# Optimization experiments

Measured on AMD Instinct MI355X. Metric: run time of the kernel, lower is better.

## Reference

```python
import jax, jax.numpy as jnp
from jax import lax
import numpy as np

GAMMA = 0.1
BIG = 1e8  # finite stand-in for +inf so grads/logsumexp stay clean

# solar radius in km; HUX propagates from 21.5 Rs (WSA inner boundary) to 1 AU (215 Rs)
RS_KM = 6.957e5
R0 = 21.5 * RS_KM
R1 = 215.0 * RS_KM
NR = 200  # radial steps (CFL ~ 0.5 for v~300 km/s, T=512)


def _hux(v_in, omega):
    """HUX-f upwind radial propagation. v_in: [B,T] km/s, omega: [B] rad/s."""
    B, T = v_in.shape
    dr = (R1 - R0) / NR
    dphi = 2.0 * jnp.pi / T  # one Carrington rotation over T samples
    om = omega[:, None]

    def step(v, _):
        dv = jnp.roll(v, -1, axis=1) - v  # periodic longitude
        v_new = v + (dr * om / (jnp.maximum(v, 1.0) * dphi)) * dv
        return v_new, None

    v_out, _ = lax.scan(step, v_in, None, length=NR)
    return v_out


def _soft_dtw(x, y, gamma):
    """Soft-DTW (Cuturi & Blondel). x,y: [B,T,1]. Returns [B]."""
    B, T, _ = x.shape
    # pairwise squared-euclidean cost  [B,T,T]
    D = jnp.sum((x[:, :, None, :] - y[:, None, :, :]) ** 2, axis=-1)
    i = jnp.arange(T)

    def softmin(a, b, c):
        return -gamma * jax.nn.logsumexp(-jnp.stack([a, b, c], 0) / gamma, axis=0)

    # anti-diagonal wavefront: r1[i] = R[i, p-1-i], r2[i] = R[i, p-2-i]
    def step(carry, p):
        r2, r1 = carry
        j = p - i
        valid = (j >= 0) & (j < T)
        d = D[:, i, jnp.clip(j, 0, T - 1)]          # [B,T] cost on diag p
        n_up = jnp.concatenate([jnp.full((B, 1), BIG, D.dtype), r1[:, :-1]], 1)   # R[i-1, p-i]
        n_left = r1                                                                # R[i, p-i-1]
        n_diag = jnp.concatenate([jnp.full((B, 1), BIG, D.dtype), r2[:, :-1]], 1)  # R[i-1, p-i-1]
        r_new = d + softmin(n_up, n_left, n_diag)
        r_new = jnp.where(valid[None, :], r_new, BIG)
        return (r1, r_new), None

    r0 = jnp.full((B, T), BIG, D.dtype).at[:, 0].set(D[:, 0, 0])  # diag p=0: R[0,0]=D[0,0]
    rm1 = jnp.full((B, T), BIG, D.dtype)
    (_, r_last), _ = lax.scan(step, (rm1, r0), jnp.arange(1, 2 * T - 1))
    return r_last[:, T - 1]  # R[T-1, T-1]


def _forward(pred_map, lat_idx, omega, omni_ts):
    B, _, H, W = pred_map.shape
    v_map = pred_map[:, 0]  # [B,H,W]
    T = lat_idx.shape[1]
    # v_in[b,t] = v_map[b, t, lat_idx[b,t]]
    v_in = jnp.take_along_axis(v_map[:, :T, :], lat_idx[:, :, None], axis=2)[..., 0]
    v_out = _hux(v_in, omega)

    v_out_scaled = (v_out - 200.0) / 1000.0
    omni_scaled = (omni_ts - 200.0) / 1000.0

    dtw_raw = _soft_dtw(omni_scaled[..., None], v_out_scaled[..., None], GAMMA)
    dtw_loss = jnp.abs(dtw_raw).mean()

    diff = v_out_scaled - omni_scaled
    rmse_loss = jnp.sqrt(jnp.sum(diff ** 2))
    mae_loss = jnp.sum(jnp.abs(diff))

    pc = v_out_scaled - v_out_scaled.mean(axis=1, keepdims=True)
    tc = omni_scaled - omni_scaled.mean(axis=1, keepdims=True)
    num = jnp.sum(pc * tc, axis=1)
    den = jnp.sqrt(jnp.sum(pc ** 2, axis=1)) * jnp.sqrt(jnp.sum(tc ** 2, axis=1))
    pcc_loss = 1.0 - (num / den).mean()

    return (v_out, mae_loss, pcc_loss, dtw_loss, rmse_loss)


def setup_inputs() -> dict:
    key = jax.random.key(0)
    k1, k2, k3, k4 = jax.random.split(key, 4)
    B, T, W = 32, 512, 128
    # realistic solar-wind speeds 300-700 km/s (keeps HUX stable and loss scaling sane)
    pred_map = 300.0 + 400.0 * jax.random.uniform(k1, (B, 1, T, W), dtype=jnp.float32)
    lat_idx = jax.random.randint(k2, (B, T), 0, W)
    omega = 2.7e-6 * (0.9 + 0.2 * jax.random.uniform(k3, (B,), dtype=jnp.float32))
    omni_ts = 300.0 + 400.0 * jax.random.uniform(k4, (B, T), dtype=jnp.float32)
    return {"pred_map": pred_map, "lat_idx": lat_idx, "omega": omega, "omni_ts": omni_ts}


def reference(pred_map, lat_idx, omega, omni_ts):
    return _forward(pred_map, lat_idx, omega, omni_ts)
```

## Files before the change

kernel.cpp:

```cpp
#include <hip/hip_runtime.h>
#include <math.h>

#define TT 512
#define NB 32
#define NRSTEP 200
#define KSC 14.4269504f
#define MAGICF 0x5CA1AB1E

#define SCHR_SCALE (-KSC * 8388608.0f)
#define SCHR_OFF   1064986823.0f

typedef float float2v __attribute__((ext_vector_type(2)));

__device__ __forceinline__ float2v pk_add(float2v a, float2v b) {
    float2v d;
    asm("v_pk_add_f32 %0, %1, %2" : "=v"(d) : "v"(a), "v"(b));
    return d;
}
__device__ __forceinline__ float2v pk_mul(float2v a, float2v b) {
    float2v d;
    asm("v_pk_mul_f32 %0, %1, %2" : "=v"(d) : "v"(a), "v"(b));
    return d;
}
__device__ __forceinline__ float2v pk_fma(float2v a, float2v b, float2v c) {
    float2v d;
    asm("v_pk_fma_f32 %0, %1, %2, %3" : "=v"(d) : "v"(a), "v"(b), "v"(c));
    return d;
}

__device__ __forceinline__ float dpp_up1_f(float x) {
    return __int_as_float(__builtin_amdgcn_update_dpp(
        0, __float_as_int(x), 0x138, 0xf, 0xf, false));
}
__device__ __forceinline__ int dpp_up1_i(int x) {
    return __builtin_amdgcn_update_dpp(0, x, 0x138, 0xf, 0xf, false);
}
__device__ __forceinline__ float dpp_dn1_f(float x) {
    return __int_as_float(__builtin_amdgcn_update_dpp(
        0, __float_as_int(x), 0x130, 0xf, 0xf, false));
}
__device__ __forceinline__ float rdlane_f(float v, int lane) {
    return __int_as_float(__builtin_amdgcn_readlane(__float_as_int(v), lane));
}
__device__ __forceinline__ float exp2i(int e) {
    return __int_as_float((e + 127) << 23);
}
__device__ __forceinline__ float2v fastrcp2(float2v a) {
    float2v r;
    r.x = __int_as_float(0x7EF311C3 - __float_as_int(a.x));
    r.y = __int_as_float(0x7EF311C3 - __float_as_int(a.y));
    return r * ((float2v){2.0f, 2.0f} - a * r);
}
__device__ __forceinline__ float2v max1_2(float2v a) {
    float2v m; m.x = fmaxf(a.x, 1.0f); m.y = fmaxf(a.y, 1.0f); return m;
}

__global__ __launch_bounds__(64, 1) void fused_kernel(
    const float* __restrict__ pred_map,
    const int*   __restrict__ lat_idx,
    const float* __restrict__ omega,
    const float* __restrict__ omni,
    float*       __restrict__ out,
    float*       __restrict__ ws)
{
    const int b    = blockIdx.x;
    const int lane = threadIdx.x;
    const int t0   = lane * 8;
    const bool lane0 = (lane == 0);

    float v[8];
    const int*   li = lat_idx + b * TT + t0;
    const float* pm = pred_map + (size_t)b * TT * 128 + (size_t)t0 * 128;
    #pragma unroll
    for (int k = 0; k < 8; ++k) v[k] = pm[k * 128 + li[k]];

    const float c = (float)(673089.75 / (2.0 * M_PI / 512.0)) * omega[b];
    const float2v c2 = {c, c};
    float2v W[4];
    W[0].x = v[0]; W[0].y = v[4];
    W[1].x = v[1]; W[1].y = v[5];
    W[2].x = v[2]; W[2].y = v[6];
    W[3].x = v[3]; W[3].y = v[7];
    #pragma unroll 1
    for (int it = 0; it < NRSTEP; ++it) {
        float rd0 = rdlane_f(W[0].x, 0);
        float vn  = dpp_dn1_f(W[0].x);
        vn = (lane == 63) ? rd0 : vn;
        float2v nb0 = W[1], nb1 = W[2], nb2 = W[3];
        float2v nb3; nb3.x = W[0].y; nb3.y = vn;
        float2v r0 = fastrcp2(max1_2(W[0]));
        float2v r1 = fastrcp2(max1_2(W[1]));
        float2v r2 = fastrcp2(max1_2(W[2]));
        float2v r3 = fastrcp2(max1_2(W[3]));
        W[0] = W[0] + c2 * r0 * (nb0 - W[0]);
        W[1] = W[1] + c2 * r1 * (nb1 - W[1]);
        W[2] = W[2] + c2 * r2 * (nb2 - W[2]);
        W[3] = W[3] + c2 * r3 * (nb3 - W[3]);
    }
    v[0] = W[0].x; v[4] = W[0].y;
    v[1] = W[1].x; v[5] = W[1].y;
    v[2] = W[2].x; v[6] = W[2].y;
    v[3] = W[3].x; v[7] = W[3].y;

    float4* o4 = (float4*)(out + b * TT + t0);
    o4[0] = make_float4(v[0], v[1], v[2], v[3]);
    o4[1] = make_float4(v[4], v[5], v[6], v[7]);

    float x[8], y8[8], y8n[8];
    const float* om = omni + b * TT + t0;
    float sx = 0.f, syy0 = 0.f;
    #pragma unroll
    for (int k = 0; k < 8; ++k) {
        x[k]   = (om[k] - 200.0f) * 1e-3f;
        y8[k]  = (v[k] - 200.0f) * 1e-3f;
        y8n[k] = -y8[k];
        sx += x[k];
        syy0 += y8[k];
    }
    #pragma unroll
    for (int m = 1; m < 64; m <<= 1) {
        sx   += __shfl_xor(sx, m, 64);
        syy0 += __shfl_xor(syy0, m, 64);
    }
    const float mx = sx * (1.0f / 512.0f);
    const float my = syy0 * (1.0f / 512.0f);

    float sab = 0.f, ssq = 0.f, snum = 0.f, sxx = 0.f, spp = 0.f;
    #pragma unroll
    for (int k = 0; k < 8; ++k) {
        float d = y8[k] - x[k];
        sab += fabsf(d);
        ssq += d * d;
        float pc = y8[k] - my;
        float tc = x[k] - mx;
        snum += pc * tc;
        sxx  += tc * tc;
        spp  += pc * pc;
    }
    #pragma unroll
    for (int m = 1; m < 64; m <<= 1) {
        sab  += __shfl_xor(sab,  m, 64);
        ssq  += __shfl_xor(ssq,  m, 64);
        snum += __shfl_xor(snum, m, 64);
        sxx  += __shfl_xor(sxx,  m, 64);
        spp  += __shfl_xor(spp,  m, 64);
    }
    const float corr = snum / (sqrtf(spp) * sqrtf(sxx));

    float2v x2[4];
    #pragma unroll
    for (int i = 0; i < 4; ++i) { x2[i].x = x[i]; x2[i].y = x[i + 4]; }
    const float2v kS2 = {SCHR_SCALE, SCHR_SCALE};
    const float2v kO2 = {SCHR_OFF, SCHR_OFF};

    float2v P[4];
    #pragma unroll
    for (int k = 0; k < 4; ++k) P[k] = (float2v){0.0f, 0.0f};
    int   E = 0;
    float c7w = 0.0f; int c7E = 0;
    float aT = 0.0f, aT2 = 0.0f;
    float pW = 0.0f;  int pE = 0;
    int   vj0 = -2 * lane;
    const float adoptW = lane0 ? 1.0f : 0.0f;

    float zA = lane0 ? y8n[0] : 0.0f;
    float zB = 0.0f;

    #pragma unroll 1
    for (int blk = 0; blk < 80; ++blk) {
        const int us  = blk < 63 ? blk : 63;
        const int us1 = blk < 62 ? blk + 1 : 63;
        float f[8];
        f[0] = rdlane_f(y8n[1], us);
        f[1] = rdlane_f(y8n[2], us);
        f[2] = rdlane_f(y8n[3], us);
        f[3] = rdlane_f(y8n[4], us);
        f[4] = rdlane_f(y8n[5], us);
        f[5] = rdlane_f(y8n[6], us);
        f[6] = rdlane_f(y8n[7], us);
        f[7] = rdlane_f(y8n[0], us1);

        #pragma unroll
        for (int q = 0; q < 8; ++q) {
            float nW  = dpp_up1_f(c7w);
            int   nEc = dpp_up1_i(c7E);

            float2v z2; z2.x = zA; z2.y = zB;
            float2v fsv[4];
            #pragma unroll
            for (int i = 0; i < 4; ++i) {
                float2v t  = pk_add(x2[i], z2);
                float2v t2 = pk_mul(t, t);
                float2v h  = pk_fma(t2, kS2, kO2);
                fsv[i].x = __int_as_float((int)h.x);
                fsv[i].y = __int_as_float((int)h.y);
            }

            const bool adopt = (vj0 == 0);
            E = adopt ? nEc : E;
            float wuA = ldexpf(nW, E - nEc);
            float wdA = ldexpf(pW, E - pE);
            wdA = adopt ? adoptW : wdA;

            float2v uc, dgn;
            uc.x  = wuA; uc.y  = aT;
            dgn.x = wdA; dgn.y = aT2;
            #pragma unroll
            for (int k = 0; k < 4; ++k) {
                float2v wl = P[k];
                float2v s  = pk_add(wl, dgn);
                float2v a  = pk_mul(fsv[k], s);
                float2v w  = pk_fma(fsv[k], uc, a);
                dgn = wl; P[k] = w; uc = w;
            }
            aT2 = aT; aT = P[3].x;

            const bool pub = ((unsigned)(vj0 - 1) < 512u);
            c7w = pub ? P[3].y : c7w;
            c7E = pub ? E : c7E;
            pW = nW; pE = nEc;

            float zn = dpp_up1_f(zB);
            zB = zA;
            zA = lane0 ? f[q] : zn;
            ++vj0;
        }

        int ebits = (int)((__float_as_uint(P[3].y) >> 23) & 255u);
        int dsh = 127 - ebits;
        dsh = dsh > 126 ? 126 : (dsh < -126 ? -126 : dsh);
        float sf = exp2i(dsh);
        E += dsh;
        float2v sf2; sf2.x = sf; sf2.y = sf;
        #pragma unroll
        for (int k = 0; k < 4; ++k) P[k] = pk_mul(P[k], sf2);
        aT *= sf; aT2 *= sf;
        c7w *= sf; c7E += dsh;
    }

    float dtwv = 0.0f;
    if (lane == 63) {
        float u = (float)c7E - __builtin_amdgcn_logf(c7w);
        dtwv = fabsf(u) * (1.0f / KSC);
    }

    float* slot = ws + 8 * b;
    if (lane == 63) slot[3] = dtwv;
    if (lane == 0) { slot[0] = sab; slot[1] = ssq; slot[2] = corr; }
    __syncthreads();
    __threadfence();
    if (lane == 0) atomicExch((int*)(slot + 4), MAGICF);

    if (b == NB - 1) {
        float m = 0.f, s = 0.f, p = 0.f, d = 0.f;
        if (lane < NB) {
            int* fl = (int*)(ws + 8 * lane + 4);
            while (atomicAdd(fl, 0) != MAGICF) { }
            __threadfence();
            float* sl = ws + 8 * lane;
            m = atomicAdd(&sl[0], 0.0f);
            s = atomicAdd(&sl[1], 0.0f);
            p = atomicAdd(&sl[2], 0.0f);
            d = atomicAdd(&sl[3], 0.0f);
        }
        #pragma unroll
        for (int mm = 1; mm < 64; mm <<= 1) {
            m += __shfl_xor(m, mm, 64);
            s += __shfl_xor(s, mm, 64);
            p += __shfl_xor(p, mm, 64);
            d += __shfl_xor(d, mm, 64);
        }
        if (lane == 0) {
            out[NB * TT + 0] = m;
            out[NB * TT + 1] = 1.0f - p * (1.0f / 32.0f);
            out[NB * TT + 2] = d * (1.0f / 32.0f);
            out[NB * TT + 3] = sqrtf(s);
        }
    }
}

extern "C" void kernel_launch(void* const* d_in, const int* in_sizes, int n_in,
                              void* d_out, int out_size, void* d_ws, size_t ws_size,
                              hipStream_t stream) {
    const float* pred_map = (const float*)d_in[0];
    const int*   lat_idx  = (const int*)d_in[1];
    const float* omega    = (const float*)d_in[2];
    const float* omni     = (const float*)d_in[3];
    float* out = (float*)d_out;
    float* ws  = (float*)d_ws;

    fused_kernel<<<NB, 64, 0, stream>>>(pred_map, lat_idx, omega, omni, out, ws);
}
```

Measured before the change: 149.0 us.

## Split soft-DTW wavefront across two waves with LDS flag handoff

The soft-DTW anti-diagonal sweep now runs on two wavefronts per block. Each wave owns 256 rows, so each lane handles 4 rows instead of 8. Wave 0 publishes its boundary-row values and exponents into shared memory, and a spin-wait flag pipelines them to wave 1, which runs several blocks behind. This halves the per-step dependent work per lane, at the cost of LDS traffic, a spin-wait, and a lag between the two waves. HUX still runs on wave 0 only.

```diff
diff --git a/kernel.cpp b/kernel.cpp
--- a/kernel.cpp
+++ b/kernel.cpp
@@ -13,19 +13,13 @@
 typedef float float2v __attribute__((ext_vector_type(2)));
 
 __device__ __forceinline__ float2v pk_add(float2v a, float2v b) {
-    float2v d;
-    asm("v_pk_add_f32 %0, %1, %2" : "=v"(d) : "v"(a), "v"(b));
-    return d;
+    float2v d; asm("v_pk_add_f32 %0, %1, %2" : "=v"(d) : "v"(a), "v"(b)); return d;
 }
 __device__ __forceinline__ float2v pk_mul(float2v a, float2v b) {
-    float2v d;
-    asm("v_pk_mul_f32 %0, %1, %2" : "=v"(d) : "v"(a), "v"(b));
-    return d;
+    float2v d; asm("v_pk_mul_f32 %0, %1, %2" : "=v"(d) : "v"(a), "v"(b)); return d;
 }
 __device__ __forceinline__ float2v pk_fma(float2v a, float2v b, float2v c) {
-    float2v d;
-    asm("v_pk_fma_f32 %0, %1, %2, %3" : "=v"(d) : "v"(a), "v"(b), "v"(c));
-    return d;
+    float2v d; asm("v_pk_fma_f32 %0, %1, %2, %3" : "=v"(d) : "v"(a), "v"(b), "v"(c)); return d;
 }
 
 __device__ __forceinline__ float dpp_up1_f(float x) {
@@ -55,7 +49,7 @@
     float2v m; m.x = fmaxf(a.x, 1.0f); m.y = fmaxf(a.y, 1.0f); return m;
 }
 
-__global__ __launch_bounds__(64, 1) void fused_kernel(
+__global__ __launch_bounds__(128, 1) void fused_kernel(
     const float* __restrict__ pred_map,
     const int*   __restrict__ lat_idx,
     const float* __restrict__ omega,
@@ -63,133 +57,159 @@
     float*       __restrict__ out,
     float*       __restrict__ ws)
 {
+    __shared__ float sYn[TT];
+    __shared__ float sX[TT];
+    __shared__ float sRW[TT];
+    __shared__ int   sRE[TT];
+    __shared__ int   sFlag;
+
+    const int tid  = threadIdx.x;
+    const int lane = tid & 63;
+    const int wv   = tid >> 6;
     const int b    = blockIdx.x;
-    const int lane = threadIdx.x;
-    const int t0   = lane * 8;
     const bool lane0 = (lane == 0);
 
-    float v[8];
-    const int*   li = lat_idx + b * TT + t0;
-    const float* pm = pred_map + (size_t)b * TT * 128 + (size_t)t0 * 128;
-    #pragma unroll
-    for (int k = 0; k < 8; ++k) v[k] = pm[k * 128 + li[k]];
-
-    const float c = (float)(673089.75 / (2.0 * M_PI / 512.0)) * omega[b];
-    const float2v c2 = {c, c};
-    float2v W[4];
-    W[0].x = v[0]; W[0].y = v[4];
-    W[1].x = v[1]; W[1].y = v[5];
-    W[2].x = v[2]; W[2].y = v[6];
-    W[3].x = v[3]; W[3].y = v[7];
-    #pragma unroll 1
-    for (int it = 0; it < NRSTEP; ++it) {
-        float rd0 = rdlane_f(W[0].x, 0);
-        float vn  = dpp_dn1_f(W[0].x);
-        vn = (lane == 63) ? rd0 : vn;
-        float2v nb0 = W[1], nb1 = W[2], nb2 = W[3];
-        float2v nb3; nb3.x = W[0].y; nb3.y = vn;
-        float2v r0 = fastrcp2(max1_2(W[0]));
-        float2v r1 = fastrcp2(max1_2(W[1]));
-        float2v r2 = fastrcp2(max1_2(W[2]));
-        float2v r3 = fastrcp2(max1_2(W[3]));
-        W[0] = W[0] + c2 * r0 * (nb0 - W[0]);
-        W[1] = W[1] + c2 * r1 * (nb1 - W[1]);
-        W[2] = W[2] + c2 * r2 * (nb2 - W[2]);
-        W[3] = W[3] + c2 * r3 * (nb3 - W[3]);
+    if (tid == 0) *(volatile int*)&sFlag = 0;
+
+    float sab = 0.f, ssq = 0.f, corr = 0.f;
+
+    if (wv == 0) {
+        const int t0 = lane * 8;
+        float v[8];
+        const int*   li = lat_idx + b * TT + t0;
+        const float* pm = pred_map + (size_t)b * TT * 128 + (size_t)t0 * 128;
+        #pragma unroll
+        for (int k = 0; k < 8; ++k) v[k] = pm[k * 128 + li[k]];
+
+        const float c = (float)(673089.75 / (2.0 * M_PI / 512.0)) * omega[b];
+        const float2v c2 = {c, c};
+        float2v W[4];
+        W[0].x = v[0]; W[0].y = v[4];
+        W[1].x = v[1]; W[1].y = v[5];
+        W[2].x = v[2]; W[2].y = v[6];
+        W[3].x = v[3]; W[3].y = v[7];
+        #pragma unroll 1
+        for (int it = 0; it < NRSTEP; ++it) {
+            float rd0 = rdlane_f(W[0].x, 0);
+            float vn  = dpp_dn1_f(W[0].x);
+            vn = (lane == 63) ? rd0 : vn;
+            float2v nb0 = W[1], nb1 = W[2], nb2 = W[3];
+            float2v nb3; nb3.x = W[0].y; nb3.y = vn;
+            float2v r0 = fastrcp2(max1_2(W[0]));
+            float2v r1 = fastrcp2(max1_2(W[1]));
+            float2v r2 = fastrcp2(max1_2(W[2]));
+            float2v r3 = fastrcp2(max1_2(W[3]));
+            W[0] = W[0] + c2 * r0 * (nb0 - W[0]);
+            W[1] = W[1] + c2 * r1 * (nb1 - W[1]);
+            W[2] = W[2] + c2 * r2 * (nb2 - W[2]);
+            W[3] = W[3] + c2 * r3 * (nb3 - W[3]);
+        }
+        v[0] = W[0].x; v[4] = W[0].y;
+        v[1] = W[1].x; v[5] = W[1].y;
+        v[2] = W[2].x; v[6] = W[2].y;
+        v[3] = W[3].x; v[7] = W[3].y;
+
+        float4* o4 = (float4*)(out + b * TT + t0);
+        o4[0] = make_float4(v[0], v[1], v[2], v[3]);
+        o4[1] = make_float4(v[4], v[5], v[6], v[7]);
+
+        float x[8], y8[8];
+        const float* om = omni + b * TT + t0;
+        float sx = 0.f, sy0 = 0.f;
+        #pragma unroll
+        for (int k = 0; k < 8; ++k) {
+            x[k]  = (om[k] - 200.0f) * 1e-3f;
+            y8[k] = (v[k] - 200.0f) * 1e-3f;
+            sYn[t0 + k] = -y8[k];
+            sX[t0 + k]  = x[k];
+            sx += x[k];
+            sy0 += y8[k];
+        }
+        #pragma unroll
+        for (int m = 1; m < 64; m <<= 1) {
+            sx  += __shfl_xor(sx, m, 64);
+            sy0 += __shfl_xor(sy0, m, 64);
+        }
+        const float mx = sx * (1.0f / 512.0f);
+        const float my = sy0 * (1.0f / 512.0f);
+        float snum = 0.f, sxx = 0.f, spp = 0.f;
+        #pragma unroll
+        for (int k = 0; k < 8; ++k) {
+            float d = y8[k] - x[k];
+            sab += fabsf(d);
+            ssq += d * d;
+            float pc = y8[k] - my;
+            float tc = x[k] - mx;
+            snum += pc * tc;
+            sxx  += tc * tc;
+            spp  += pc * pc;
+        }
+        #pragma unroll
+        for (int m = 1; m < 64; m <<= 1) {
+            sab  += __shfl_xor(sab,  m, 64);
+            ssq  += __shfl_xor(ssq,  m, 64);
+            snum += __shfl_xor(snum, m, 64);
+            sxx  += __shfl_xor(sxx,  m, 64);
+            spp  += __shfl_xor(spp,  m, 64);
+        }
+        corr = snum / (sqrtf(spp) * sqrtf(sxx));
     }
-    v[0] = W[0].x; v[4] = W[0].y;
-    v[1] = W[1].x; v[5] = W[1].y;
-    v[2] = W[2].x; v[6] = W[2].y;
-    v[3] = W[3].x; v[7] = W[3].y;
-
-    float4* o4 = (float4*)(out + b * TT + t0);
-    o4[0] = make_float4(v[0], v[1], v[2], v[3]);
-    o4[1] = make_float4(v[4], v[5], v[6], v[7]);
-
-    float x[8], y8[8], y8n[8];
-    const float* om = omni + b * TT + t0;
-    float sx = 0.f, syy0 = 0.f;
-    #pragma unroll
-    for (int k = 0; k < 8; ++k) {
-        x[k]   = (om[k] - 200.0f) * 1e-3f;
-        y8[k]  = (v[k] - 200.0f) * 1e-3f;
-        y8n[k] = -y8[k];
-        sx += x[k];
-        syy0 += y8[k];
-    }
-    #pragma unroll
-    for (int m = 1; m < 64; m <<= 1) {
-        sx   += __shfl_xor(sx, m, 64);
-        syy0 += __shfl_xor(syy0, m, 64);
-    }
-    const float mx = sx * (1.0f / 512.0f);
-    const float my = syy0 * (1.0f / 512.0f);
-
-    float sab = 0.f, ssq = 0.f, snum = 0.f, sxx = 0.f, spp = 0.f;
-    #pragma unroll
-    for (int k = 0; k < 8; ++k) {
-        float d = y8[k] - x[k];
-        sab += fabsf(d);
-        ssq += d * d;
-        float pc = y8[k] - my;
-        float tc = x[k] - mx;
-        snum += pc * tc;
-        sxx  += tc * tc;
-        spp  += pc * pc;
-    }
-    #pragma unroll
-    for (int m = 1; m < 64; m <<= 1) {
-        sab  += __shfl_xor(sab,  m, 64);
-        ssq  += __shfl_xor(ssq,  m, 64);
-        snum += __shfl_xor(snum, m, 64);
-        sxx  += __shfl_xor(sxx,  m, 64);
-        spp  += __shfl_xor(spp,  m, 64);
-    }
-    const float corr = snum / (sqrtf(spp) * sqrtf(sxx));
-
-    float2v x2[4];
-    #pragma unroll
-    for (int i = 0; i < 4; ++i) { x2[i].x = x[i]; x2[i].y = x[i + 4]; }
+    __syncthreads();
+
+    const int rbase = (wv << 8) + (lane << 2);
+    float2v X2[2];
+    X2[0].x = sX[rbase];     X2[0].y = sX[rbase + 2];
+    X2[1].x = sX[rbase + 1]; X2[1].y = sX[rbase + 3];
     const float2v kS2 = {SCHR_SCALE, SCHR_SCALE};
     const float2v kO2 = {SCHR_OFF, SCHR_OFF};
 
-    float2v P[4];
-    #pragma unroll
-    for (int k = 0; k < 4; ++k) P[k] = (float2v){0.0f, 0.0f};
+    float2v P[2];
+    P[0] = (float2v){0.0f, 0.0f};
+    P[1] = (float2v){0.0f, 0.0f};
     int   E = 0;
     float c7w = 0.0f; int c7E = 0;
     float aT = 0.0f, aT2 = 0.0f;
     float pW = 0.0f;  int pE = 0;
     int   vj0 = -2 * lane;
-    const float adoptW = lane0 ? 1.0f : 0.0f;
-
-    float zA = lane0 ? y8n[0] : 0.0f;
+    const float adoptW = (tid == 0) ? 1.0f : 0.0f;
+    const bool  w1l0   = (tid == 64);
+    float zA = lane0 ? sYn[0] : 0.0f;
     float zB = 0.0f;
 
     #pragma unroll 1
     for (int blk = 0; blk < 80; ++blk) {
-        const int us  = blk < 63 ? blk : 63;
-        const int us1 = blk < 62 ? blk + 1 : 63;
-        float f[8];
-        f[0] = rdlane_f(y8n[1], us);
-        f[1] = rdlane_f(y8n[2], us);
-        f[2] = rdlane_f(y8n[3], us);
-        f[3] = rdlane_f(y8n[4], us);
-        f[4] = rdlane_f(y8n[5], us);
-        f[5] = rdlane_f(y8n[6], us);
-        f[6] = rdlane_f(y8n[7], us);
-        f[7] = rdlane_f(y8n[0], us1);
+        float f[8], rw[8]; int rEv[8];
+        if (wv) {
+            int need = blk + 17; need = need > 80 ? 80 : need;
+            while (*(volatile int*)&sFlag < need) { }
+            __threadfence_block();
+            #pragma unroll
+            for (int q = 0; q < 8; ++q) {
+                int cc = 8 * blk + q; cc = cc > 511 ? 511 : cc;
+                rw[q] = sRW[cc]; rEv[q] = sRE[cc];
+            }
+        } else {
+            #pragma unroll
+            for (int q = 0; q < 8; ++q) { rw[q] = 0.0f; rEv[q] = 0; }
+        }
+        #pragma unroll
+        for (int q = 0; q < 8; ++q) {
+            int cc = 8 * blk + 1 + q; cc = cc > 511 ? 511 : cc;
+            f[q] = sYn[cc];
+        }
 
         #pragma unroll
         for (int q = 0; q < 8; ++q) {
             float nW  = dpp_up1_f(c7w);
             int   nEc = dpp_up1_i(c7E);
+            nW  = w1l0 ? rw[q]  : nW;
+            nEc = w1l0 ? rEv[q] : nEc;
 
             float2v z2; z2.x = zA; z2.y = zB;
-            float2v fsv[4];
+            float2v fsv[2];
             #pragma unroll
-            for (int i = 0; i < 4; ++i) {
-                float2v t  = pk_add(x2[i], z2);
+            for (int i = 0; i < 2; ++i) {
+                float2v t  = pk_add(X2[i], z2);
                 float2v t2 = pk_mul(t, t);
                 float2v h  = pk_fma(t2, kS2, kO2);
                 fsv[i].x = __int_as_float((int)h.x);
@@ -206,19 +226,24 @@
             uc.x  = wuA; uc.y  = aT;
             dgn.x = wdA; dgn.y = aT2;
             #pragma unroll
-            for (int k = 0; k < 4; ++k) {
+            for (int k = 0; k < 2; ++k) {
                 float2v wl = P[k];
                 float2v s  = pk_add(wl, dgn);
                 float2v a  = pk_mul(fsv[k], s);
                 float2v w  = pk_fma(fsv[k], uc, a);
                 dgn = wl; P[k] = w; uc = w;
             }
-            aT2 = aT; aT = P[3].x;
+            aT2 = aT; aT = P[1].x;
 
             const bool pub = ((unsigned)(vj0 - 1) < 512u);
-            c7w = pub ? P[3].y : c7w;
+            c7w = pub ? P[1].y : c7w;
             c7E = pub ? E : c7E;
             pW = nW; pE = nEc;
+
+            int col = 8 * blk + q - 127;
+            if (tid == 63 && (unsigned)col < 512u) {
+                sRW[col] = c7w; sRE[col] = c7E;
+            }
 
             float zn = dpp_up1_f(zB);
             zB = zA;
@@ -226,38 +251,43 @@
             ++vj0;
         }
 
-        int ebits = (int)((__float_as_uint(P[3].y) >> 23) & 255u);
+        int ebits = (int)((__float_as_uint(P[1].y) >> 23) & 255u);
         int dsh = 127 - ebits;
         dsh = dsh > 126 ? 126 : (dsh < -126 ? -126 : dsh);
         float sf = exp2i(dsh);
         E += dsh;
         float2v sf2; sf2.x = sf; sf2.y = sf;
-        #pragma unroll
-        for (int k = 0; k < 4; ++k) P[k] = pk_mul(P[k], sf2);
+        P[0] = pk_mul(P[0], sf2);
+        P[1] = pk_mul(P[1], sf2);
         aT *= sf; aT2 *= sf;
         c7w *= sf; c7E += dsh;
+
+        if (tid == 63) {
+            __threadfence_block();
+            *(volatile int*)&sFlag = blk + 1;
+        }
     }
 
     float dtwv = 0.0f;
-    if (lane == 63) {
+    if (tid == 127) {
         float u = (float)c7E - __builtin_amdgcn_logf(c7w);
         dtwv = fabsf(u) * (1.0f / KSC);
     }
 
     float* slot = ws + 8 * b;
-    if (lane == 63) slot[3] = dtwv;
-    if (lane == 0) { slot[0] = sab; slot[1] = ssq; slot[2] = corr; }
+    if (tid == 127) slot[3] = dtwv;
+    if (tid == 0) { slot[0] = sab; slot[1] = ssq; slot[2] = corr; }
     __syncthreads();
     __threadfence();
-    if (lane == 0) atomicExch((int*)(slot + 4), MAGICF);
-
-    if (b == NB - 1) {
+    if (tid == 0) atomicExch((int*)(slot + 4), MAGICF);
+
+    if (b == NB - 1 && tid < 64) {
         float m = 0.f, s = 0.f, p = 0.f, d = 0.f;
-        if (lane < NB) {
-            int* fl = (int*)(ws + 8 * lane + 4);
+        if (tid < NB) {
+            int* fl = (int*)(ws + 8 * tid + 4);
             while (atomicAdd(fl, 0) != MAGICF) { }
             __threadfence();
-            float* sl = ws + 8 * lane;
+            float* sl = ws + 8 * tid;
             m = atomicAdd(&sl[0], 0.0f);
             s = atomicAdd(&sl[1], 0.0f);
             p = atomicAdd(&sl[2], 0.0f);
@@ -270,7 +300,7 @@
             p += __shfl_xor(p, mm, 64);
             d += __shfl_xor(d, mm, 64);
         }
-        if (lane == 0) {
+        if (tid == 0) {
             out[NB * TT + 0] = m;
             out[NB * TT + 1] = 1.0f - p * (1.0f / 32.0f);
             out[NB * TT + 2] = d * (1.0f / 32.0f);
@@ -289,5 +319,5 @@
     float* out = (float*)d_out;
     float* ws  = (float*)d_ws;
 
-    fused_kernel<<<NB, 64, 0, stream>>>(pred_map, lat_idx, omega, omni, out, ws);
-}
+    fused_kernel<<<NB, 128, 0, stream>>>(pred_map, lat_idx, omega, omni, out, ws);
+}
```

After: 185.1 us. 24.3% more time.
